# Kernel optimization log

Hardware: AMD Instinct MI355X
Metric: run time of the kernel (lower is better)

Reference implementation:

```python
import jax, jax.numpy as jnp
import numpy as np

B, NH, NQ, NK, D = 2, 12, 2048, 2048, 64


def setup_inputs() -> dict:
    k0 = jax.random.key(0)
    k1, k2, k3, k4 = jax.random.split(k0, 4)
    return {
        "query": jax.random.normal(k1, (B, NH, NQ, D), dtype=jnp.float32),
        "key": jax.random.normal(k2, (B, NH, NK, D), dtype=jnp.float32),
        "value": jax.random.normal(k3, (B, NH, NK, D), dtype=jnp.float32),
        "mask": jnp.zeros((B, 1, NQ, NK), dtype=jnp.float32),
        "bias": jax.random.normal(k4, (NQ + NK + 1, NH), dtype=jnp.float32) * 0.02,
    }


def reference(query, key, value, mask, bias):
    head_size = query.shape[-1]
    nq = query.shape[-2]
    nk = key.shape[-2]
    # scores [B, H, Q, K]
    qk = jnp.einsum("bhqd,bhkd->bhqk", query, key) / jnp.sqrt(jnp.float32(head_size)).astype(query.dtype)
    # relative position bias: table [(nq+nk+1), nh] gathered at pos_q - pos_k + nk
    pos_qk = jnp.arange(nq)[:, None] - jnp.arange(nk)[None, :] + nk  # [Q, K]
    bias_qk = bias[pos_qk]                      # [Q, K, H]
    bias_qk = jnp.transpose(bias_qk, (2, 0, 1))[None]  # [1, H, Q, K]
    qk = qk + bias_qk + mask
    attn = jax.nn.softmax(qk, axis=-1)
    return jnp.einsum("bhqk,bhkd->bhqd", attn, value)
```

## Files before the change

### kernel.cpp

```cpp
#include <hip/hip_runtime.h>

#define NB  2
#define NH  12
#define NQ  2048
#define NKV 2048
#define DH  64
#define KVB 64
#define BH  (NB * NH)

#define L2E 1.44269504088896f
#define QSCL (0.125f * L2E)

typedef __attribute__((ext_vector_type(8))) short bf16x8;
typedef __attribute__((ext_vector_type(4))) short bf16x4;
typedef __attribute__((ext_vector_type(4))) float f32x4;
typedef __attribute__((ext_vector_type(2))) unsigned short u16x2;

#define EXP2F(x) __builtin_amdgcn_exp2f(x)

#define WS_KB   0u
#define WS_VT   6291456u
#define WS_NEED 12582912u

__device__ __forceinline__ unsigned short f2bf(float f) {
    unsigned int u = __float_as_uint(f);
    u += 0x7FFFu + ((u >> 16) & 1u);
    return (unsigned short)(u >> 16);
}
__device__ __forceinline__ float bf2f(unsigned short h) {
    return __uint_as_float((unsigned int)h << 16);
}
__device__ __forceinline__ int permk6(int k6) {
    return (k6 & 32) + ((k6 & 12) << 1) + ((k6 & 16) >> 2) + (k6 & 3);
}

__global__ __launch_bounds__(256)
void conv_kv(const float* __restrict__ K, const float* __restrict__ V,
             unsigned short* __restrict__ Kb, unsigned short* __restrict__ Vt)
{
    const int tid = threadIdx.x;
    const int kvt = blockIdx.x & 31;
    const int bh  = blockIdx.x >> 5;
    const int kv0 = kvt * 64;

    const float* ksrc = K + ((size_t)bh * NKV + kv0) * DH;
    const float* vsrc = V + ((size_t)bh * NKV + kv0) * DH;
    unsigned short* kdst = Kb + ((size_t)bh * NKV + kv0) * DH;
    unsigned short* vdst = Vt + (size_t)bh * DH * NKV + kv0;

    __shared__ float Ts[64][65];

#pragma unroll
    for (int p = 0; p < 2; ++p) {
        const int ch = p * 256 + tid;
        const int row = ch >> 3, c8 = (ch & 7) * 8;
        const float4 f0 = *(const float4*)(ksrc + (size_t)row * DH + c8);
        const float4 f1 = *(const float4*)(ksrc + (size_t)row * DH + c8 + 4);
        bf16x8 o;
        o[0] = (short)f2bf(f0.x); o[1] = (short)f2bf(f0.y);
        o[2] = (short)f2bf(f0.z); o[3] = (short)f2bf(f0.w);
        o[4] = (short)f2bf(f1.x); o[5] = (short)f2bf(f1.y);
        o[6] = (short)f2bf(f1.z); o[7] = (short)f2bf(f1.w);
        *(bf16x8*)(kdst + (size_t)row * DH + c8) = o;
    }
#pragma unroll
    for (int p = 0; p < 4; ++p) {
        const int fi = p * 1024 + tid * 4;
        const int row = fi >> 6, col = fi & 63;
        const float4 f = *(const float4*)(vsrc + (size_t)row * DH + col);
        Ts[row][col] = f.x; Ts[row][col + 1] = f.y;
        Ts[row][col + 2] = f.z; Ts[row][col + 3] = f.w;
    }
    __syncthreads();
#pragma unroll
    for (int p = 0; p < 2; ++p) {
        const int ch = p * 256 + tid;
        const int d = ch >> 3, c8 = (ch & 7) * 8;
        bf16x8 o;
#pragma unroll
        for (int j = 0; j < 8; ++j) o[j] = (short)f2bf(Ts[c8 + j][d]);
        unsigned short* vrow = vdst + (size_t)d * NKV;
        *(uint2*)(vrow + permk6(c8))     = ((const uint2*)&o)[0];
        *(uint2*)(vrow + permk6(c8 + 4)) = ((const uint2*)&o)[1];
    }
}

#define ARENA_BYTES 45312
#define KS_OFF 8448
#define VS_OFF 26880
#define BUF_STRIDE 9216

__global__ __launch_bounds__(512, 2)
void attn_fwd(const unsigned short* __restrict__ Kb, const unsigned short* __restrict__ Vt,
              const float* __restrict__ Q, const float* __restrict__ M,
              const float* __restrict__ Bias, float* __restrict__ O)
{
    const int tid  = threadIdx.x;
    const int w    = tid >> 6;
    const int wq   = w >> 1;
    const int wk   = w & 1;
    const int lane = tid & 63;
    const int l16  = lane & 15;
    const int g    = lane >> 4;

    const int qt = blockIdx.x & 31;
    const int bh = blockIdx.x >> 5;
    const int h  = bh % NH;
    const int b  = bh / NH;
    const int q0 = qt * 64;

    __shared__ __align__(16) char arena[ARENA_BYTES];
    unsigned short* bias2 = (unsigned short*)arena;

    for (int x = tid; x < 2112; x += 512) {
        const unsigned short v = f2bf(L2E * Bias[(size_t)(q0 + 1 + x) * NH + h]);
        bias2[2111 - x] = v;
        if (x <= 2110) bias2[2112 + 2110 - x] = v;
    }

    const float* qptr = Q + ((size_t)bh * NQ + q0 + wq * 16 + l16) * DH;
    bf16x8 qa[2];
#pragma unroll
    for (int dc = 0; dc < 2; ++dc) {
        const float4 f0 = *(const float4*)(qptr + dc * 32 + g * 8);
        const float4 f1 = *(const float4*)(qptr + dc * 32 + g * 8 + 4);
        qa[dc][0] = (short)f2bf(f0.x * QSCL); qa[dc][1] = (short)f2bf(f0.y * QSCL);
        qa[dc][2] = (short)f2bf(f0.z * QSCL); qa[dc][3] = (short)f2bf(f0.w * QSCL);
        qa[dc][4] = (short)f2bf(f1.x * QSCL); qa[dc][5] = (short)f2bf(f1.y * QSCL);
        qa[dc][6] = (short)f2bf(f1.z * QSCL); qa[dc][7] = (short)f2bf(f1.w * QSCL);
    }

    f32x4 o[4];
#pragma unroll
    for (int nt = 0; nt < 4; ++nt) { o[nt][0]=0.f; o[nt][1]=0.f; o[nt][2]=0.f; o[nt][3]=0.f; }
    float m_r = -1e30f;
    float l_r = 0.f;

    const unsigned short* kbB = Kb + (size_t)bh * NKV * DH;
    const unsigned short* vtB = Vt + (size_t)bh * DH * NKV;
    const float* mbase = M + (size_t)b * NQ * NKV
                           + (size_t)(q0 + wq * 16 + l16) * NKV + wk * 32 + g * 4;

    const int srow = tid >> 3, sc8 = (tid & 7) * 8;
    const int ldoff = srow * 144 + sc8 * 2;

    bf16x8 krB, vrB;
    float4 mr4[2], mrn4[2];
    krB = *(const bf16x8*)(kbB + (size_t)srow * DH + sc8);
    vrB = *(const bf16x8*)(vtB + (size_t)srow * NKV + sc8);
#pragma unroll
    for (int nt = 0; nt < 2; ++nt) mr4[nt] = *(const float4*)(mbase + nt * 16);

    *(bf16x8*)(arena + KS_OFF + ldoff) = krB;
    *(bf16x8*)(arena + VS_OFF + ldoff) = vrB;
    krB = *(const bf16x8*)(kbB + (size_t)(64 + srow) * DH + sc8);
    vrB = *(const bf16x8*)(vtB + (size_t)srow * NKV + 64 + sc8);
    __syncthreads();

    int cur = 0;
    for (int t = 0; t < NKV / KVB; ++t) {
        const int kv0 = t * KVB;
        const int tn  = ((t + 1) & (NKV / KVB - 1)) * KVB;
        const int t2  = ((t + 2) & (NKV / KVB - 1)) * KVB;
        const int nxt = cur ^ 1;

        *(bf16x8*)(arena + KS_OFF + nxt * BUF_STRIDE + ldoff) = krB;
        *(bf16x8*)(arena + VS_OFF + nxt * BUF_STRIDE + ldoff) = vrB;
        krB = *(const bf16x8*)(kbB + (size_t)(t2 + srow) * DH + sc8);
        vrB = *(const bf16x8*)(vtB + (size_t)srow * NKV + t2 + sc8);
#pragma unroll
        for (int nt = 0; nt < 2; ++nt) mrn4[nt] = *(const float4*)(mbase + tn + nt * 16);

        const unsigned short (*Ks)[72] = (const unsigned short(*)[72])(arena + KS_OFF + cur * BUF_STRIDE);
        const unsigned short (*Vs)[72] = (const unsigned short(*)[72])(arena + VS_OFF + cur * BUF_STRIDE);

        f32x4 s[2];
        __builtin_amdgcn_s_setprio(1);
#pragma unroll
        for (int nt = 0; nt < 2; ++nt) {
            f32x4 acc; acc[0]=0.f; acc[1]=0.f; acc[2]=0.f; acc[3]=0.f;
            const int kvrow = wk * 32 + nt * 16 + l16;
            const bf16x8 kb0 = *(const bf16x8*)(&Ks[kvrow][g * 8]);
            const bf16x8 kb1 = *(const bf16x8*)(&Ks[kvrow][32 + g * 8]);
            acc = __builtin_amdgcn_mfma_f32_16x16x32_bf16(kb0, qa[0], acc, 0, 0, 0);
            acc = __builtin_amdgcn_mfma_f32_16x16x32_bf16(kb1, qa[1], acc, 0, 0, 0);
            s[nt] = acc;
        }
        __builtin_amdgcn_s_setprio(0);

        bf16x8 va2[4];
#pragma unroll
        for (int nt = 0; nt < 4; ++nt)
            va2[nt] = *(const bf16x8*)(&Vs[nt * 16 + l16][wk * 32 + g * 8]);

        const int ib0 = (wq * 16 + l16) - (kv0 + wk * 32 + g * 4) + 2047;
#pragma unroll
        for (int nt = 0; nt < 2; ++nt) {
            const int j0 = 2111 - (ib0 - nt * 16);
            const int r  = j0 & 1;
            const unsigned short* bp = bias2 + r * 2112 + (j0 - r);
            const u16x2 b01 = *(const u16x2*)(bp);
            const u16x2 b23 = *(const u16x2*)(bp + 2);
            s[nt][0] += __fmaf_rn(nt ? mr4[1].x : mr4[0].x, L2E, bf2f(b01[0]));
            s[nt][1] += __fmaf_rn(nt ? mr4[1].y : mr4[0].y, L2E, bf2f(b01[1]));
            s[nt][2] += __fmaf_rn(nt ? mr4[1].z : mr4[0].z, L2E, bf2f(b23[0]));
            s[nt][3] += __fmaf_rn(nt ? mr4[1].w : mr4[0].w, L2E, bf2f(b23[1]));
        }

        const float x0  = fmaxf(fmaxf(s[0][0], s[0][1]), s[0][2]);
        const float x1  = fmaxf(fmaxf(s[0][3], s[1][0]), s[1][1]);
        const float x2  = fmaxf(s[1][2], s[1][3]);
        const float lmx = fmaxf(fmaxf(x0, x1), x2);
        if (__any(lmx > m_r + 8.0f)) {
            float mx = lmx;
            mx = fmaxf(mx, __shfl_xor(mx, 16));
            mx = fmaxf(mx, __shfl_xor(mx, 32));
            const float mn = fmaxf(m_r, mx);
            const float alpha = EXP2F(m_r - mn);
            m_r = mn;
            l_r *= alpha;
#pragma unroll
            for (int nt = 0; nt < 4; ++nt) {
                o[nt][0] *= alpha; o[nt][1] *= alpha;
                o[nt][2] *= alpha; o[nt][3] *= alpha;
            }
        }
        f32x4 pv[2];
#pragma unroll
        for (int nt = 0; nt < 2; ++nt) {
            pv[nt][0] = EXP2F(s[nt][0] - m_r);
            pv[nt][1] = EXP2F(s[nt][1] - m_r);
            pv[nt][2] = EXP2F(s[nt][2] - m_r);
            pv[nt][3] = EXP2F(s[nt][3] - m_r);
        }
        l_r += ((pv[0][0] + pv[0][1]) + (pv[0][2] + pv[0][3]))
             + ((pv[1][0] + pv[1][1]) + (pv[1][2] + pv[1][3]));

        mr4[0] = mrn4[0]; mr4[1] = mrn4[1];

        union { unsigned u[4]; bf16x8 v; } pb8;
        asm("v_cvt_pk_bf16_f32 %0, %1, %2" : "=v"(pb8.u[0]) : "v"(pv[0][0]), "v"(pv[0][1]));
        asm("v_cvt_pk_bf16_f32 %0, %1, %2" : "=v"(pb8.u[1]) : "v"(pv[0][2]), "v"(pv[0][3]));
        asm("v_cvt_pk_bf16_f32 %0, %1, %2" : "=v"(pb8.u[2]) : "v"(pv[1][0]), "v"(pv[1][1]));
        asm("v_cvt_pk_bf16_f32 %0, %1, %2" : "=v"(pb8.u[3]) : "v"(pv[1][2]), "v"(pv[1][3]));

        __builtin_amdgcn_s_setprio(1);
#pragma unroll
        for (int nt = 0; nt < 4; ++nt)
            o[nt] = __builtin_amdgcn_mfma_f32_16x16x32_bf16(va2[nt], pb8.v, o[nt], 0, 0, 0);
        __builtin_amdgcn_s_setprio(0);

        __syncthreads();
        cur = nxt;
    }

    l_r += __shfl_xor(l_r, 16);
    l_r += __shfl_xor(l_r, 32);

    float (*mO)[64][17] = (float(*)[64][17])(arena + KS_OFF);
    float* mML          = (float*)(arena + KS_OFF + 17408);

    __syncthreads();
    if (wk == 1) {
#pragma unroll
        for (int nt = 0; nt < 4; ++nt) {
#pragma unroll
            for (int reg = 0; reg < 4; ++reg)
                mO[wq][nt * 16 + g * 4 + reg][l16] = o[nt][reg];
        }
        if (g == 0) {
            mML[wq * 16 + l16]      = m_r;
            mML[64 + wq * 16 + l16] = l_r;
        }
    }
    __syncthreads();
    if (wk == 0) {
        const float m1 = mML[wq * 16 + l16];
        const float l1 = mML[64 + wq * 16 + l16];
        const float mn = fmaxf(m_r, m1);
        const float a0 = EXP2F(m_r - mn);
        const float a1 = EXP2F(m1 - mn);
        const float inv = 1.f / (l_r * a0 + l1 * a1);
        float* obase = O + ((size_t)bh * NQ + q0 + wq * 16 + l16) * DH;
#pragma unroll
        for (int nt = 0; nt < 4; ++nt) {
            float4 ov;
            ov.x = (o[nt][0] * a0 + mO[wq][nt * 16 + g * 4 + 0][l16] * a1) * inv;
            ov.y = (o[nt][1] * a0 + mO[wq][nt * 16 + g * 4 + 1][l16] * a1) * inv;
            ov.z = (o[nt][2] * a0 + mO[wq][nt * 16 + g * 4 + 2][l16] * a1) * inv;
            ov.w = (o[nt][3] * a0 + mO[wq][nt * 16 + g * 4 + 3][l16] * a1) * inv;
            *(float4*)(obase + nt * 16 + g * 4) = ov;
        }
    }
}

__global__ __launch_bounds__(256, 3)
void attn_full(const float* __restrict__ Q, const float* __restrict__ K,
               const float* __restrict__ V, const float* __restrict__ M,
               const float* __restrict__ Bias, float* __restrict__ O)
{
    const int tid  = threadIdx.x;
    const int wv   = tid >> 6;
    const int lane = tid & 63;
    const int l16  = lane & 15;
    const int g    = lane >> 4;

    const int qt = blockIdx.x & 31;
    const int h  = (blockIdx.x >> 5) % NH;
    const int b  = blockIdx.x / (32 * NH);
    const int q0 = qt * 64;

    __shared__ float bias_s[2112];
    __shared__ unsigned short Ks[64][72];
    __shared__ unsigned short Vs[64][72];
    __shared__ unsigned short Ps[4][16][72];

    for (int i = tid; i < 2112; i += 256)
        bias_s[i] = Bias[(size_t)(q0 + 1 + i) * NH + h];

    const float* qptr = Q + (((size_t)b * NH + h) * NQ + q0 + wv * 16 + l16) * DH;
    bf16x8 qa[2];
#pragma unroll
    for (int dc = 0; dc < 2; ++dc) {
        const float4 f0 = *(const float4*)(qptr + dc * 32 + g * 8);
        const float4 f1 = *(const float4*)(qptr + dc * 32 + g * 8 + 4);
        qa[dc][0] = (short)f2bf(f0.x); qa[dc][1] = (short)f2bf(f0.y);
        qa[dc][2] = (short)f2bf(f0.z); qa[dc][3] = (short)f2bf(f0.w);
        qa[dc][4] = (short)f2bf(f1.x); qa[dc][5] = (short)f2bf(f1.y);
        qa[dc][6] = (short)f2bf(f1.z); qa[dc][7] = (short)f2bf(f1.w);
    }

    f32x4 o[4];
#pragma unroll
    for (int nt = 0; nt < 4; ++nt) { o[nt][0]=0.f; o[nt][1]=0.f; o[nt][2]=0.f; o[nt][3]=0.f; }
    float m_r[4] = {-1e30f, -1e30f, -1e30f, -1e30f};
    float l_r[4] = {0.f, 0.f, 0.f, 0.f};

    const float* kbase = K + ((size_t)b * NH + h) * NKV * DH;
    const float* vbase = V + ((size_t)b * NH + h) * NKV * DH;
    const float* mrow[4];
#pragma unroll
    for (int r = 0; r < 4; ++r)
        mrow[r] = M + (size_t)b * NQ * NKV + (size_t)(q0 + wv * 16 + g * 4 + r) * NKV + l16;

    const int r0 = tid >> 4, c0 = (tid & 15) * 4;

    float4 kr[4], vr[4];
    float  mr[4][4];
#pragma unroll
    for (int i = 0; i < 4; ++i) {
        kr[i] = *(const float4*)(kbase + (size_t)(i * 16 + r0) * DH + c0);
        vr[i] = *(const float4*)(vbase + (size_t)(i * 16 + r0) * DH + c0);
    }
#pragma unroll
    for (int r = 0; r < 4; ++r)
#pragma unroll
        for (int nt = 0; nt < 4; ++nt) mr[r][nt] = mrow[r][nt * 16];

    for (int t = 0; t < NKV / 64; ++t) {
        const int kv0 = t * 64;
        const int kvn = ((t + 1) & 31) * 64;

        __syncthreads();
#pragma unroll
        for (int i = 0; i < 4; ++i) {
            unsigned short* dst = &Ks[i * 16 + r0][c0];
            dst[0] = f2bf(kr[i].x); dst[1] = f2bf(kr[i].y);
            dst[2] = f2bf(kr[i].z); dst[3] = f2bf(kr[i].w);
        }
#pragma unroll
        for (int i = 0; i < 4; ++i) {
            const int rr = i * 16 + r0;
            Vs[c0 + 0][rr] = f2bf(vr[i].x); Vs[c0 + 1][rr] = f2bf(vr[i].y);
            Vs[c0 + 2][rr] = f2bf(vr[i].z); Vs[c0 + 3][rr] = f2bf(vr[i].w);
        }
#pragma unroll
        for (int i = 0; i < 4; ++i) {
            kr[i] = *(const float4*)(kbase + (size_t)(kvn + i * 16 + r0) * DH + c0);
            vr[i] = *(const float4*)(vbase + (size_t)(kvn + i * 16 + r0) * DH + c0);
        }
        __syncthreads();

        f32x4 s[4];
#pragma unroll
        for (int nt = 0; nt < 4; ++nt) {
            f32x4 acc; acc[0]=0.f; acc[1]=0.f; acc[2]=0.f; acc[3]=0.f;
            const bf16x8 kb0 = *(const bf16x8*)(&Ks[nt * 16 + l16][g * 8]);
            const bf16x8 kb1 = *(const bf16x8*)(&Ks[nt * 16 + l16][32 + g * 8]);
            acc = __builtin_amdgcn_mfma_f32_16x16x32_bf16(qa[0], kb0, acc, 0, 0, 0);
            acc = __builtin_amdgcn_mfma_f32_16x16x32_bf16(qa[1], kb1, acc, 0, 0, 0);
            s[nt] = acc;
        }

#pragma unroll
        for (int r = 0; r < 4; ++r) {
            const int qr = wv * 16 + g * 4 + r;
#pragma unroll
            for (int nt = 0; nt < 4; ++nt) {
                float x = s[nt][r] * 0.125f + mr[r][nt];
                x += bias_s[qr - (kv0 + nt * 16 + l16) + 2047];
                s[nt][r] = x;
            }
            float mx = fmaxf(fmaxf(s[0][r], s[1][r]), fmaxf(s[2][r], s[3][r]));
            mx = fmaxf(mx, __shfl_xor(mx, 1));
            mx = fmaxf(mx, __shfl_xor(mx, 2));
            mx = fmaxf(mx, __shfl_xor(mx, 4));
            mx = fmaxf(mx, __shfl_xor(mx, 8));
            const float mo = m_r[r];
            const float mn = fmaxf(mo, mx);
            m_r[r] = mn;
            const float alpha = __expf(mo - mn);
            float p[4], rs = 0.f;
#pragma unroll
            for (int nt = 0; nt < 4; ++nt) { p[nt] = __expf(s[nt][r] - mn); rs += p[nt]; }
            rs += __shfl_xor(rs, 1);
            rs += __shfl_xor(rs, 2);
            rs += __shfl_xor(rs, 4);
            rs += __shfl_xor(rs, 8);
            l_r[r] = l_r[r] * alpha + rs;
#pragma unroll
            for (int nt = 0; nt < 4; ++nt) o[nt][r] *= alpha;
#pragma unroll
            for (int nt = 0; nt < 4; ++nt)
                Ps[wv][g * 4 + r][nt * 16 + l16] = f2bf(p[nt]);
        }

#pragma unroll
        for (int r = 0; r < 4; ++r)
#pragma unroll
            for (int nt = 0; nt < 4; ++nt) mr[r][nt] = mrow[r][kvn + nt * 16];

#pragma unroll
        for (int kc = 0; kc < 2; ++kc) {
            const bf16x8 pa = *(const bf16x8*)(&Ps[wv][l16][kc * 32 + g * 8]);
#pragma unroll
            for (int nt = 0; nt < 4; ++nt) {
                const bf16x8 vb = *(const bf16x8*)(&Vs[nt * 16 + l16][kc * 32 + g * 8]);
                o[nt] = __builtin_amdgcn_mfma_f32_16x16x32_bf16(pa, vb, o[nt], 0, 0, 0);
            }
        }
    }

    float* obase = O + (((size_t)b * NH + h) * NQ + q0 + wv * 16) * DH;
#pragma unroll
    for (int r = 0; r < 4; ++r) {
        const float inv = 1.f / l_r[r];
#pragma unroll
        for (int nt = 0; nt < 4; ++nt)
            obase[(size_t)(g * 4 + r) * DH + nt * 16 + l16] = o[nt][r] * inv;
    }
}

extern "C" void kernel_launch(void* const* d_in, const int* in_sizes, int n_in,
                              void* d_out, int out_size, void* d_ws, size_t ws_size,
                              hipStream_t stream) {
    const float* Q    = (const float*)d_in[0];
    const float* K    = (const float*)d_in[1];
    const float* V    = (const float*)d_in[2];
    const float* M    = (const float*)d_in[3];
    const float* Bias = (const float*)d_in[4];
    float* O = (float*)d_out;

    if (ws_size >= (size_t)WS_NEED) {
        unsigned short* Kb = (unsigned short*)((char*)d_ws + WS_KB);
        unsigned short* Vt = (unsigned short*)((char*)d_ws + WS_VT);
        conv_kv<<<dim3(BH * 32), dim3(256), 0, stream>>>(K, V, Kb, Vt);
        attn_fwd<<<dim3(BH * 32), dim3(512), 0, stream>>>(Kb, Vt, Q, M, Bias, O);
    } else {
        attn_full<<<dim3(BH * 32), dim3(256), 0, stream>>>(Q, K, V, M, Bias, O);
    }
}
```

Baseline: 78.84 us.

## Pre-swizzle V into MFMA fragment layout and load directly to registers

```diff
diff --git a/kernel.cpp b/kernel.cpp
--- a/kernel.cpp
+++ b/kernel.cpp
@@ -19,7 +19,7 @@
 #define EXP2F(x) __builtin_amdgcn_exp2f(x)
 
 #define WS_KB   0u
-#define WS_VT   6291456u
+#define WS_VG   6291456u
 #define WS_NEED 12582912u
 
 __device__ __forceinline__ unsigned short f2bf(float f) {
@@ -30,13 +30,10 @@
 __device__ __forceinline__ float bf2f(unsigned short h) {
     return __uint_as_float((unsigned int)h << 16);
 }
-__device__ __forceinline__ int permk6(int k6) {
-    return (k6 & 32) + ((k6 & 12) << 1) + ((k6 & 16) >> 2) + (k6 & 3);
-}
 
 __global__ __launch_bounds__(256)
 void conv_kv(const float* __restrict__ K, const float* __restrict__ V,
-             unsigned short* __restrict__ Kb, unsigned short* __restrict__ Vt)
+             unsigned short* __restrict__ Kb, unsigned short* __restrict__ Vg2)
 {
     const int tid = threadIdx.x;
     const int kvt = blockIdx.x & 31;
@@ -46,7 +43,7 @@
     const float* ksrc = K + ((size_t)bh * NKV + kv0) * DH;
     const float* vsrc = V + ((size_t)bh * NKV + kv0) * DH;
     unsigned short* kdst = Kb + ((size_t)bh * NKV + kv0) * DH;
-    unsigned short* vdst = Vt + (size_t)bh * DH * NKV + kv0;
+    unsigned short* vg2T = Vg2 + (size_t)bh * NKV * DH + (size_t)kvt * 4096;
 
     __shared__ float Ts[64][65];
 
@@ -72,26 +69,34 @@
         Ts[row][col + 2] = f.z; Ts[row][col + 3] = f.w;
     }
     __syncthreads();
-#pragma unroll
-    for (int p = 0; p < 2; ++p) {
-        const int ch = p * 256 + tid;
-        const int d = ch >> 3, c8 = (ch & 7) * 8;
-        bf16x8 o;
-#pragma unroll
-        for (int j = 0; j < 8; ++j) o[j] = (short)f2bf(Ts[c8 + j][d]);
-        unsigned short* vrow = vdst + (size_t)d * NKV;
-        *(uint2*)(vrow + permk6(c8))     = ((const uint2*)&o)[0];
-        *(uint2*)(vrow + permk6(c8 + 4)) = ((const uint2*)&o)[1];
-    }
-}
-
-#define ARENA_BYTES 45312
+    {
+        const int ci0 = tid * 2;
+        const int g0  = ci0 & 3;
+        const int l   = (ci0 >> 2) & 15;
+        const int nt  = (ci0 >> 6) & 3;
+        const int wkk = (ci0 >> 8) & 1;
+        const int d   = nt * 16 + l;
+        bf16x8 o2[2];
+#pragma unroll
+        for (int gg = 0; gg < 2; ++gg) {
+            const int g = g0 + gg;
+#pragma unroll
+            for (int j2 = 0; j2 < 8; ++j2) {
+                const int kv = wkk * 32 + ((j2 >> 2) << 4) + g * 4 + (j2 & 3);
+                o2[gg][j2] = (short)f2bf(Ts[kv][d]);
+            }
+        }
+        *(bf16x8*)(vg2T + tid * 16)     = o2[0];
+        *(bf16x8*)(vg2T + tid * 16 + 8) = o2[1];
+    }
+}
+
+#define ARENA_BYTES 26880
 #define KS_OFF 8448
-#define VS_OFF 26880
 #define BUF_STRIDE 9216
 
 __global__ __launch_bounds__(512, 2)
-void attn_fwd(const unsigned short* __restrict__ Kb, const unsigned short* __restrict__ Vt,
+void attn_fwd(const unsigned short* __restrict__ Kb, const unsigned short* __restrict__ Vg2,
               const float* __restrict__ Q, const float* __restrict__ M,
               const float* __restrict__ Bias, float* __restrict__ O)
 {
@@ -103,8 +108,8 @@
     const int l16  = lane & 15;
     const int g    = lane >> 4;
 
-    const int qt = blockIdx.x & 31;
-    const int bh = blockIdx.x >> 5;
+    const int bh = blockIdx.x % BH;
+    const int qt = blockIdx.x / BH;
     const int h  = bh % NH;
     const int b  = bh / NH;
     const int q0 = qt * 64;
@@ -137,24 +142,25 @@
     float l_r = 0.f;
 
     const unsigned short* kbB = Kb + (size_t)bh * NKV * DH;
-    const unsigned short* vtB = Vt + (size_t)bh * DH * NKV;
+    const unsigned short* vg2W = Vg2 + (size_t)bh * NKV * DH
+                               + wk * 2048 + l16 * 32 + g * 8;
     const float* mbase = M + (size_t)b * NQ * NKV
                            + (size_t)(q0 + wq * 16 + l16) * NKV + wk * 32 + g * 4;
 
     const int srow = tid >> 3, sc8 = (tid & 7) * 8;
     const int ldoff = srow * 144 + sc8 * 2;
 
-    bf16x8 krB, vrB;
+    bf16x8 krB;
     float4 mr4[2], mrn4[2];
+    bf16x8 va_c[4], va_n[4];
     krB = *(const bf16x8*)(kbB + (size_t)srow * DH + sc8);
-    vrB = *(const bf16x8*)(vtB + (size_t)srow * NKV + sc8);
 #pragma unroll
     for (int nt = 0; nt < 2; ++nt) mr4[nt] = *(const float4*)(mbase + nt * 16);
-
+#pragma unroll
+    for (int nt = 0; nt < 4; ++nt)
+        va_c[nt] = *(const bf16x8*)(vg2W + nt * 512);
     *(bf16x8*)(arena + KS_OFF + ldoff) = krB;
-    *(bf16x8*)(arena + VS_OFF + ldoff) = vrB;
     krB = *(const bf16x8*)(kbB + (size_t)(64 + srow) * DH + sc8);
-    vrB = *(const bf16x8*)(vtB + (size_t)srow * NKV + 64 + sc8);
     __syncthreads();
 
     int cur = 0;
@@ -165,14 +171,14 @@
         const int nxt = cur ^ 1;
 
         *(bf16x8*)(arena + KS_OFF + nxt * BUF_STRIDE + ldoff) = krB;
-        *(bf16x8*)(arena + VS_OFF + nxt * BUF_STRIDE + ldoff) = vrB;
         krB = *(const bf16x8*)(kbB + (size_t)(t2 + srow) * DH + sc8);
-        vrB = *(const bf16x8*)(vtB + (size_t)srow * NKV + t2 + sc8);
 #pragma unroll
         for (int nt = 0; nt < 2; ++nt) mrn4[nt] = *(const float4*)(mbase + tn + nt * 16);
+#pragma unroll
+        for (int nt = 0; nt < 4; ++nt)
+            va_n[nt] = *(const bf16x8*)(vg2W + (size_t)(tn >> 6) * 4096 + nt * 512);
 
         const unsigned short (*Ks)[72] = (const unsigned short(*)[72])(arena + KS_OFF + cur * BUF_STRIDE);
-        const unsigned short (*Vs)[72] = (const unsigned short(*)[72])(arena + VS_OFF + cur * BUF_STRIDE);
 
         f32x4 s[2];
         __builtin_amdgcn_s_setprio(1);
@@ -187,11 +193,6 @@
             s[nt] = acc;
         }
         __builtin_amdgcn_s_setprio(0);
-
-        bf16x8 va2[4];
-#pragma unroll
-        for (int nt = 0; nt < 4; ++nt)
-            va2[nt] = *(const bf16x8*)(&Vs[nt * 16 + l16][wk * 32 + g * 8]);
 
         const int ib0 = (wq * 16 + l16) - (kv0 + wk * 32 + g * 4) + 2047;
 #pragma unroll
@@ -247,8 +248,11 @@
         __builtin_amdgcn_s_setprio(1);
 #pragma unroll
         for (int nt = 0; nt < 4; ++nt)
-            o[nt] = __builtin_amdgcn_mfma_f32_16x16x32_bf16(va2[nt], pb8.v, o[nt], 0, 0, 0);
+            o[nt] = __builtin_amdgcn_mfma_f32_16x16x32_bf16(va_c[nt], pb8.v, o[nt], 0, 0, 0);
         __builtin_amdgcn_s_setprio(0);
+
+#pragma unroll
+        for (int nt = 0; nt < 4; ++nt) va_c[nt] = va_n[nt];
 
         __syncthreads();
         cur = nxt;
@@ -462,10 +466,10 @@
     float* O = (float*)d_out;
 
     if (ws_size >= (size_t)WS_NEED) {
-        unsigned short* Kb = (unsigned short*)((char*)d_ws + WS_KB);
-        unsigned short* Vt = (unsigned short*)((char*)d_ws + WS_VT);
-        conv_kv<<<dim3(BH * 32), dim3(256), 0, stream>>>(K, V, Kb, Vt);
-        attn_fwd<<<dim3(BH * 32), dim3(512), 0, stream>>>(Kb, Vt, Q, M, Bias, O);
+        unsigned short* Kb  = (unsigned short*)((char*)d_ws + WS_KB);
+        unsigned short* Vg2 = (unsigned short*)((char*)d_ws + WS_VG);
+        conv_kv<<<dim3(BH * 32), dim3(256), 0, stream>>>(K, V, Kb, Vg2);
+        attn_fwd<<<dim3(BH * 32), dim3(512), 0, stream>>>(Kb, Vg2, Q, M, Bias, O);
     } else {
         attn_full<<<dim3(BH * 32), dim3(256), 0, stream>>>(Q, K, V, M, Bias, O);
     }
```

After: 112.3 us. 42.4% more time.
